# Optimization experiments

Measured on AMD Instinct MI355X. Metric: run time of the kernel, lower is better.

The kernel has to match this reference:

```python
import jax, jax.numpy as jnp
import numpy as np

EPS = 1e-5

def _act_quant(x):
    # per-token absmax int8 quantization (BitNet b1.58)
    scale = 127.0 / jnp.clip(jnp.max(jnp.abs(x), axis=-1, keepdims=True), EPS)
    return jnp.clip(jnp.round(x * scale), -128.0, 127.0) / scale

def _weight_quant(w):
    # per-tensor absmean ternary quantization {-1, 0, +1}
    scale = 1.0 / jnp.clip(jnp.mean(jnp.abs(w)), EPS)
    return jnp.clip(jnp.round(w * scale), -1.0, 1.0) / scale

def _bitlinear(x, w):
    # STE: forward uses quantized values, gradient passes through
    xq = x + jax.lax.stop_gradient(_act_quant(x) - x)
    wq = w + jax.lax.stop_gradient(_weight_quant(w) - w)
    # torch Linear: y = x @ W.T, W is [out, in]
    return jnp.einsum('bsd,od->bso', xq, wq)

def setup_inputs() -> dict:
    key = jax.random.key(0)
    k1, k2, k3, k4 = jax.random.split(key, 4)
    B, S, D = 8, 2048, 512
    x = jax.random.normal(k1, (B, S, D), dtype=jnp.float32)
    s = (1.0 / D) ** 0.5
    Wq = jax.random.normal(k2, (D, D), dtype=jnp.float32) * s
    Wk = jax.random.normal(k3, (D, D), dtype=jnp.float32) * s
    Wv = jax.random.normal(k4, (D, D), dtype=jnp.float32) * s
    return {"x": x, "Wq": Wq, "Wk": Wk, "Wv": Wv}

def reference(x, Wq, Wk, Wv):
    B, S, D = x.shape
    q = _bitlinear(x, Wq)
    k = _bitlinear(x, Wk)
    v = _bitlinear(x, Wv)
    # NOTE: original scales by batch_size**-0.5 (faithful to source)
    scores = jnp.einsum('bqd,bkd->bqk', q, k) * (B ** -0.5)
    causal = jnp.tril(jnp.ones((S, S), dtype=bool))  # tril[:S, :S]
    scores = jnp.where(causal, scores, -jnp.inf)
    attn = jax.nn.softmax(scores, axis=-1)
    return jnp.einsum('bqk,bkd->bqd', attn, v)
```

## Files before the change

### kernel.cpp

```cpp
#include <hip/hip_runtime.h>
#include <cstdint>
#include <cstddef>

#define BATCH 8
#define SEQ   2048
#define DDIM  512
#define NROW  (BATCH*SEQ)
#define KPACK (DDIM/4)
#define EPSQ  1e-5f
#define FSCALE 0.35355339059327373f

typedef _Float16 half8 __attribute__((ext_vector_type(8)));
typedef _Float16 half4 __attribute__((ext_vector_type(4)));
typedef float    f32x4 __attribute__((ext_vector_type(4)));
typedef int      i32x4 __attribute__((ext_vector_type(4)));

static constexpr size_t OFF_M   = 0;
static constexpr size_t OFF_WP  = 256;
static constexpr size_t OFF_XQ  = OFF_WP + (size_t)3*KPACK*DDIM*4;
static constexpr size_t OFF_SX  = OFF_XQ + (size_t)NROW*KPACK*4;
static constexpr size_t OFF_QKV = OFF_SX + (size_t)NROW*4;
static constexpr size_t OFF_PO  = OFF_QKV + (size_t)3*NROW*DDIM*2;
static constexpr size_t OFF_PM  = OFF_PO + (size_t)512*64*512*4;
static constexpr size_t OFF_PL  = OFF_PM + (size_t)1024*32*4;

__device__ __forceinline__ int q8(float v, float s) {
  int i = (int)rintf(v * s);
  i = i < -128 ? -128 : (i > 127 ? 127 : i);
  return i & 0xff;
}

__device__ __forceinline__ void gld_lds16(const _Float16* g, _Float16* l) {
  __builtin_amdgcn_global_load_lds(
      (const __attribute__((address_space(1))) void*)g,
      (__attribute__((address_space(3))) void*)l, 16, 0, 0);
}

__global__ __launch_bounds__(256) void wsum_kernel(
    const float* __restrict__ Wq, const float* __restrict__ Wk,
    const float* __restrict__ Wv, float* __restrict__ mw) {
  const float* W = blockIdx.y == 0 ? Wq : (blockIdx.y == 1 ? Wk : Wv);
  __shared__ float red[256];
  const float4* p = (const float4*)(W + blockIdx.x * 8192);
  float s = 0.f;
  #pragma unroll
  for (int i = 0; i < 8; i++) {
    float4 a = p[i * 256 + threadIdx.x];
    s += fabsf(a.x) + fabsf(a.y) + fabsf(a.z) + fabsf(a.w);
  }
  red[threadIdx.x] = s;
  __syncthreads();
  for (int w = 128; w > 0; w >>= 1) {
    if ((int)threadIdx.x < w) red[threadIdx.x] += red[threadIdx.x + w];
    __syncthreads();
  }
  if (threadIdx.x == 0) atomicAdd(&mw[blockIdx.y], red[0]);
}

__global__ __launch_bounds__(256) void wquant_kernel(
    const float* __restrict__ Wq, const float* __restrict__ Wk,
    const float* __restrict__ Wv, const float* __restrict__ mw,
    int* __restrict__ wp) {
  int idx = blockIdx.x * 256 + threadIdx.x;
  int mat = idx >> 16;
  int local = idx & 0xFFFF;
  int o  = local >> 7;
  int k4 = local & 127;
  const float* W = mat == 0 ? Wq : (mat == 1 ? Wk : Wv);
  float mean = mw[mat] * (1.0f / 262144.0f);
  float scale = 1.0f / fmaxf(mean, EPSQ);
  float4 w4 = *(const float4*)(W + (size_t)o * DDIM + k4 * 4);
  int t0 = (int)rintf(w4.x * scale); t0 = t0 < -1 ? -1 : (t0 > 1 ? 1 : t0);
  int t1 = (int)rintf(w4.y * scale); t1 = t1 < -1 ? -1 : (t1 > 1 ? 1 : t1);
  int t2 = (int)rintf(w4.z * scale); t2 = t2 < -1 ? -1 : (t2 > 1 ? 1 : t2);
  int t3 = (int)rintf(w4.w * scale); t3 = t3 < -1 ? -1 : (t3 > 1 ? 1 : t3);
  int packed = (t0 & 0xff) | ((t1 & 0xff) << 8) | ((t2 & 0xff) << 16) | ((t3 & 0xff) << 24);
  wp[((size_t)mat * DDIM + o) * KPACK + k4] = packed;
}

__global__ __launch_bounds__(256) void aquant_kernel(
    const float* __restrict__ x, int* __restrict__ xq, float* __restrict__ sx) {
  int wid = threadIdx.x >> 6, lane = threadIdx.x & 63;
  int row = blockIdx.x * 4 + wid;
  const float* xr = x + (size_t)row * DDIM;
  float4 a = ((const float4*)xr)[lane];
  float4 b = ((const float4*)xr)[64 + lane];
  float amax = fmaxf(fmaxf(fmaxf(fabsf(a.x), fabsf(a.y)), fmaxf(fabsf(a.z), fabsf(a.w))),
                     fmaxf(fmaxf(fabsf(b.x), fabsf(b.y)), fmaxf(fabsf(b.z), fabsf(b.w))));
  for (int off = 32; off > 0; off >>= 1) amax = fmaxf(amax, __shfl_xor(amax, off, 64));
  float aa = fmaxf(amax, EPSQ);
  float scale = 127.0f / aa;
  int p0 = q8(a.x, scale) | (q8(a.y, scale) << 8) | (q8(a.z, scale) << 16) | (q8(a.w, scale) << 24);
  int p1 = q8(b.x, scale) | (q8(b.y, scale) << 8) | (q8(b.z, scale) << 16) | (q8(b.w, scale) << 24);
  xq[(size_t)row * KPACK + lane]      = p0;
  xq[(size_t)row * KPACK + 64 + lane] = p1;
  if (lane == 0) sx[row] = aa * (1.0f / 127.0f);
}

__global__ __launch_bounds__(256, 2) void qkv_gemm_kernel(
    const int* __restrict__ xq, const int* __restrict__ wp,
    const float* __restrict__ sx, const float* __restrict__ mw,
    _Float16* __restrict__ qkv) {
  __shared__ __align__(16) int xs[64][132];
  __shared__ __align__(16) int bs[64][132];
  __shared__ float sxs[64];

  const int tid  = threadIdx.x;
  const int w    = tid >> 6;
  const int lane = tid & 63;
  const int quad = lane >> 4;
  const int col  = lane & 15;

  const int r0g = blockIdx.x * 64;
  const int n0  = blockIdx.y * 64;
  const int mat = blockIdx.z;

  {
    const i32x4* src = (const i32x4*)(xq + (size_t)r0g * KPACK);
    #pragma unroll
    for (int i = 0; i < 8; i++) {
      int e = i * 256 + tid;
      int row = e >> 5, u = e & 31;
      *(i32x4*)&xs[row][u * 4] = src[e];
    }
  }
  {
    const i32x4* src = (const i32x4*)(wp + ((size_t)mat * DDIM + n0) * KPACK);
    #pragma unroll
    for (int i = 0; i < 8; i++) {
      int e = i * 256 + tid;
      int c = e >> 5, u = e & 31;
      *(i32x4*)&bs[c][u * 4] = src[e];
    }
  }
  if (tid < 64) sxs[tid] = sx[r0g + tid];
  __syncthreads();

  i32x4 acc[4];
  #pragma unroll
  for (int rt = 0; rt < 4; rt++) acc[rt] = (i32x4)(0);

  #pragma unroll
  for (int s = 0; s < 8; s++) {
    i32x4 bf = *(const i32x4*)&bs[w * 16 + col][s * 16 + quad * 4];
    #pragma unroll
    for (int rt = 0; rt < 4; rt++) {
      i32x4 af = *(const i32x4*)&xs[rt * 16 + col][s * 16 + quad * 4];
      acc[rt] = __builtin_amdgcn_mfma_i32_16x16x64_i8(af, bf, acc[rt], 0, 0, 0);
    }
  }

  const float mval = fmaxf(mw[mat] * (1.0f / 262144.0f), EPSQ);
  const int nw = n0 + w * 16 + col;

  if (mat < 2) {
    _Float16* outb = qkv + (size_t)mat * NROW * DDIM;
    #pragma unroll
    for (int rt = 0; rt < 4; rt++) {
      #pragma unroll
      for (int reg = 0; reg < 4; reg++) {
        int rowl = rt * 16 + quad * 4 + reg;
        outb[(size_t)(r0g + rowl) * DDIM + nw] =
            (_Float16)((float)acc[rt][reg] * sxs[rowl] * mval);
      }
    }
  } else {
    _Float16* vT = qkv + (size_t)2 * NROW * DDIM;
    #pragma unroll
    for (int rt = 0; rt < 4; rt++) {
      half4 hv;
      #pragma unroll
      for (int reg = 0; reg < 4; reg++) {
        int rowl = rt * 16 + quad * 4 + reg;
        hv[reg] = (_Float16)((float)acc[rt][reg] * sxs[rowl] * mval);
      }
      int r = r0g + rt * 16 + quad * 4;
      int b = r >> 11, kt = (r & 2047) >> 5, kin = r & 31;
      *(half4*)(vT + ((((size_t)b * 64 + kt) * 512 + nw) * 32 + kin)) = hv;
    }
  }
}

__global__ __launch_bounds__(256, 2) void flash_kernel(
    const _Float16* __restrict__ q, const _Float16* __restrict__ k,
    const _Float16* __restrict__ vT, _Float16* __restrict__ po,
    float* __restrict__ pm, float* __restrict__ pl) {
  __shared__ __align__(16) _Float16 Ksh[32][520];
  __shared__ __align__(16) float    PsS[32 * 33];
  __shared__ __align__(16) _Float16 Pf[32 * 40];
  __shared__ float alpha_l[32];

  const int tid  = threadIdx.x;
  const int w    = tid >> 6;
  const int lane = tid & 63;
  const int quad = lane >> 4;
  const int col  = lane & 15;
  const int rt   = w & 1;
  const int kh   = w >> 1;
  const int smrow = tid >> 3;
  const int sme   = tid & 7;
  const int d0  = w * 128;

  const int bb = blockIdx.x & 7;
  const int r  = blockIdx.x >> 3;
  const int h  = r < 64 ? 0 : 1;
  const int qt = r < 64 ? r : 127 - r;
  const int nT = h == 0 ? (qt / 2 + 1) : ((qt + 1) / 2);
  const int slot = (qt * 8 + bb) * 2 + h;

  const int qrow0 = qt * 32;
  const size_t bbase = (size_t)bb * SEQ * DDIM;
  const _Float16* kb_p = k + bbase;
  const _Float16* vt_p = vT + (size_t)bb * 64 * 512 * 32;

  half8 qfrag[16];
  {
    const _Float16* qrow_p = q + bbase + (size_t)(qrow0 + rt * 16 + col) * DDIM;
    #pragma unroll
    for (int s = 0; s < 16; s++)
      qfrag[s] = *(const half8*)(qrow_p + s * 32 + quad * 8);
  }

  float m_run = -INFINITY, l_run = 0.f;
  f32x4 o[2][8];
  #pragma unroll
  for (int a = 0; a < 2; a++)
    #pragma unroll
    for (int b2 = 0; b2 < 8; b2++) o[a][b2] = (f32x4)(0.f);

  if (nT > 0) {
    #pragma unroll
    for (int i = 0; i < 8; i++)
      gld_lds16(kb_p + (size_t)(h * 32 + w * 8 + i) * DDIM + lane * 8,
                &Ksh[w * 8 + i][0]);
    __syncthreads();
  }

  for (int t = 0; t < nT; t++) {
    const int kt  = 2 * t + h;
    const int kb0 = kt * 32;

    {
      f32x4 c = (f32x4)(0.f);
      __builtin_amdgcn_s_setprio(1);
      #pragma unroll
      for (int s = 0; s < 16; s++) {
        half8 b = *(const half8*)&Ksh[kh * 16 + col][s * 32 + quad * 8];
        c = __builtin_amdgcn_mfma_f32_16x16x32_f16(qfrag[s], b, c, 0, 0, 0);
      }
      __builtin_amdgcn_s_setprio(0);
      #pragma unroll
      for (int reg = 0; reg < 4; reg++)
        PsS[(rt * 16 + quad * 4 + reg) * 33 + kh * 16 + col] = c[reg];
    }
    __syncthreads();

    if (t + 1 < nT) {
      const int kb1 = (2 * (t + 1) + h) * 32;
      #pragma unroll
      for (int i = 0; i < 8; i++)
        gld_lds16(kb_p + (size_t)(kb1 + w * 8 + i) * DDIM + lane * 8,
                  &Ksh[w * 8 + i][0]);
    }

    {
      const int qrow = qrow0 + smrow;
      float sv[4];
      #pragma unroll
      for (int i = 0; i < 4; i++) {
        float s = PsS[smrow * 33 + sme * 4 + i] * FSCALE;
        if (kb0 + sme * 4 + i > qrow) s = -INFINITY;
        sv[i] = s;
      }
      float mx = fmaxf(fmaxf(sv[0], sv[1]), fmaxf(sv[2], sv[3]));
      #pragma unroll
      for (int m = 1; m <= 4; m <<= 1) mx = fmaxf(mx, __shfl_xor(mx, m, 64));
      float mn = fmaxf(m_run, mx);
      float mnc = fmaxf(mn, -1e30f);
      float al = __expf(m_run - mnc);
      half4 p4;
      float rs = 0.f;
      #pragma unroll
      for (int i = 0; i < 4; i++) {
        float p = __expf(sv[i] - mnc);
        rs += p;
        p4[i] = (_Float16)p;
      }
      #pragma unroll
      for (int m = 1; m <= 4; m <<= 1) rs += __shfl_xor(rs, m, 64);
      l_run = l_run * al + rs;
      m_run = mn;
      *(half4*)&Pf[smrow * 40 + sme * 4] = p4;
      if (sme == 0) alpha_l[smrow] = al;
    }
    __syncthreads();

    {
      half8 ap[2];
      f32x4 af[2];
      #pragma unroll
      for (int r2 = 0; r2 < 2; r2++) {
        ap[r2] = *(const half8*)&Pf[(r2 * 16 + col) * 40 + quad * 8];
        af[r2] = *(const f32x4*)&alpha_l[r2 * 16 + quad * 4];
      }
      #pragma unroll
      for (int r2 = 0; r2 < 2; r2++)
        #pragma unroll
        for (int ct = 0; ct < 8; ct++)
          o[r2][ct] *= af[r2];
      const _Float16* vtile = vt_p + (size_t)kt * 512 * 32;
      __builtin_amdgcn_s_setprio(1);
      #pragma unroll
      for (int ct = 0; ct < 8; ct++) {
        int R = d0 + ct * 16 + col;
        half8 bv = *(const half8*)(vtile + (size_t)R * 32 + quad * 8);
        #pragma unroll
        for (int r2 = 0; r2 < 2; r2++)
          o[r2][ct] = __builtin_amdgcn_mfma_f32_16x16x32_f16(ap[r2], bv, o[r2][ct], 0, 0, 0);
      }
      __builtin_amdgcn_s_setprio(0);
    }
  }

  if (sme == 0) {
    pm[slot * 32 + smrow] = m_run;
    pl[slot * 32 + smrow] = l_run;
  }
  {
    _Float16* pob = po + (size_t)slot * 32 * 512;
    #pragma unroll
    for (int r2 = 0; r2 < 2; r2++) {
      #pragma unroll
      for (int ct = 0; ct < 8; ct++) {
        #pragma unroll
        for (int e = 0; e < 4; e++) {
          __builtin_nontemporal_store(
              (_Float16)o[r2][ct][e],
              &pob[(size_t)(r2 * 16 + quad * 4 + e) * 512 + d0 + ct * 16 + col]);
        }
      }
    }
  }
}

__global__ __launch_bounds__(256) void merge_kernel(
    const _Float16* __restrict__ po, const float* __restrict__ pm,
    const float* __restrict__ pl, float* __restrict__ out) {
  __shared__ float w0s[32], w1s[32], dns[32];
  const int tid = threadIdx.x;
  const int qt = blockIdx.x, b = blockIdx.y;
  const int slot0 = (qt * 8 + b) * 2;
  const int slot1 = slot0 + 1;

  if (tid < 32) {
    float m0 = pm[slot0 * 32 + tid], m1 = pm[slot1 * 32 + tid];
    float l0 = pl[slot0 * 32 + tid], l1 = pl[slot1 * 32 + tid];
    float ms = fmaxf(m0, m1);
    float a0 = __expf(m0 - ms);
    float a1 = __expf(m1 - ms);
    w0s[tid] = a0;
    w1s[tid] = a1;
    dns[tid] = 1.0f / (a0 * l0 + a1 * l1);
  }
  __syncthreads();

  const half8* p0 = (const half8*)(po + (size_t)slot0 * 32 * 512);
  const half8* p1 = (const half8*)(po + (size_t)slot1 * 32 * 512);
  f32x4* op = (f32x4*)(out + ((size_t)b * SEQ + qt * 32) * 512);
  #pragma unroll 4
  for (int j = 0; j < 8; j++) {
    int e = j * 256 + tid;
    int row = e >> 6;
    half8 a = __builtin_nontemporal_load(p0 + e);
    half8 c = __builtin_nontemporal_load(p1 + e);
    float w0 = w0s[row], w1 = w1s[row], dn = dns[row];
    f32x4 r0, r1;
    #pragma unroll
    for (int u = 0; u < 4; u++) r0[u] = ((float)a[u] * w0 + (float)c[u] * w1) * dn;
    #pragma unroll
    for (int u = 0; u < 4; u++) r1[u] = ((float)a[4 + u] * w0 + (float)c[4 + u] * w1) * dn;
    op[e * 2]     = r0;
    op[e * 2 + 1] = r1;
  }
}

extern "C" void kernel_launch(void* const* d_in, const int* in_sizes, int n_in,
                              void* d_out, int out_size, void* d_ws, size_t ws_size,
                              hipStream_t stream) {
  const float* x  = (const float*)d_in[0];
  const float* Wq = (const float*)d_in[1];
  const float* Wk = (const float*)d_in[2];
  const float* Wv = (const float*)d_in[3];
  float* out = (float*)d_out;
  char* ws = (char*)d_ws;

  float* mw  = (float*)(ws + OFF_M);
  int*   wp  = (int*)(ws + OFF_WP);
  int*   xq  = (int*)(ws + OFF_XQ);
  float* sx  = (float*)(ws + OFF_SX);
  _Float16* qkv = (_Float16*)(ws + OFF_QKV);
  _Float16* qf  = qkv;
  _Float16* kf  = qkv + (size_t)NROW * DDIM;
  _Float16* vTf = qkv + 2 * (size_t)NROW * DDIM;
  _Float16* po = (_Float16*)(ws + OFF_PO);
  float* pm = (float*)(ws + OFF_PM);
  float* pl = (float*)(ws + OFF_PL);

  hipMemsetAsync(mw, 0, 16, stream);
  wsum_kernel<<<dim3(32, 3), 256, 0, stream>>>(Wq, Wk, Wv, mw);
  wquant_kernel<<<768, 256, 0, stream>>>(Wq, Wk, Wv, mw, wp);
  aquant_kernel<<<4096, 256, 0, stream>>>(x, xq, sx);
  qkv_gemm_kernel<<<dim3(256, 8, 3), 256, 0, stream>>>(xq, wp, sx, mw, qkv);
  flash_kernel<<<dim3(1024), 256, 0, stream>>>(qf, kf, vTf, po, pm, pl);
  merge_kernel<<<dim3(64, 8), 256, 0, stream>>>(po, pm, pl, out);
}
```

Baseline: 239.4 us.

## Fuse split-KV merge into flash kernel and double-buffer swizzled K tiles

```diff
diff --git a/kernel.cpp b/kernel.cpp
--- a/kernel.cpp
+++ b/kernel.cpp
@@ -15,14 +15,15 @@
 typedef float    f32x4 __attribute__((ext_vector_type(4)));
 typedef int      i32x4 __attribute__((ext_vector_type(4)));
 
-static constexpr size_t OFF_M   = 0;
-static constexpr size_t OFF_WP  = 256;
-static constexpr size_t OFF_XQ  = OFF_WP + (size_t)3*KPACK*DDIM*4;
-static constexpr size_t OFF_SX  = OFF_XQ + (size_t)NROW*KPACK*4;
-static constexpr size_t OFF_QKV = OFF_SX + (size_t)NROW*4;
-static constexpr size_t OFF_PO  = OFF_QKV + (size_t)3*NROW*DDIM*2;
-static constexpr size_t OFF_PM  = OFF_PO + (size_t)512*64*512*4;
-static constexpr size_t OFF_PL  = OFF_PM + (size_t)1024*32*4;
+static constexpr size_t OFF_M     = 0;
+static constexpr size_t OFF_FLAGS = 64;
+static constexpr size_t OFF_WP    = 4096;
+static constexpr size_t OFF_XQ    = OFF_WP + (size_t)3*KPACK*DDIM*4;
+static constexpr size_t OFF_SX    = OFF_XQ + (size_t)NROW*KPACK*4;
+static constexpr size_t OFF_QKV   = OFF_SX + (size_t)NROW*4;
+static constexpr size_t OFF_PO    = OFF_QKV + (size_t)3*NROW*DDIM*2;
+static constexpr size_t OFF_PM    = OFF_PO + (size_t)1024*32*512*2;
+static constexpr size_t OFF_PL    = OFF_PM + (size_t)1024*32*4;
 
 __device__ __forceinline__ int q8(float v, float s) {
   int i = (int)rintf(v * s);
@@ -184,11 +185,13 @@
 __global__ __launch_bounds__(256, 2) void flash_kernel(
     const _Float16* __restrict__ q, const _Float16* __restrict__ k,
     const _Float16* __restrict__ vT, _Float16* __restrict__ po,
-    float* __restrict__ pm, float* __restrict__ pl) {
-  __shared__ __align__(16) _Float16 Ksh[32][520];
+    float* __restrict__ pm, float* __restrict__ pl,
+    int* __restrict__ flags, float* __restrict__ out) {
+  __shared__ __align__(16) _Float16 Ksh[2][32][512];
   __shared__ __align__(16) float    PsS[32 * 33];
   __shared__ __align__(16) _Float16 Pf[32 * 40];
   __shared__ float alpha_l[32];
+  __shared__ int role;
 
   const int tid  = threadIdx.x;
   const int w    = tid >> 6;
@@ -231,21 +234,38 @@
   if (nT > 0) {
     #pragma unroll
     for (int i = 0; i < 8; i++)
-      gld_lds16(kb_p + (size_t)(h * 32 + w * 8 + i) * DDIM + lane * 8,
-                &Ksh[w * 8 + i][0]);
+      gld_lds16(kb_p + (size_t)(h * 32 + w * 8 + i) * DDIM + (lane ^ i) * 8,
+                &Ksh[0][w * 8 + i][0]);
     __syncthreads();
   }
 
   for (int t = 0; t < nT; t++) {
+    const int cur = t & 1;
     const int kt  = 2 * t + h;
     const int kb0 = kt * 32;
+
+    if (t + 1 < nT) {
+      const int kb1 = (2 * t + 2 + h) * 32;
+      #pragma unroll
+      for (int i = 0; i < 8; i++)
+        gld_lds16(kb_p + (size_t)(kb1 + w * 8 + i) * DDIM + (lane ^ i) * 8,
+                  &Ksh[cur ^ 1][w * 8 + i][0]);
+    }
+    half8 vreg[8];
+    {
+      const _Float16* vtile = vt_p + (size_t)kt * 512 * 32;
+      #pragma unroll
+      for (int ct = 0; ct < 8; ct++)
+        vreg[ct] = *(const half8*)(vtile + (size_t)(d0 + ct * 16 + col) * 32 + quad * 8);
+    }
 
     {
       f32x4 c = (f32x4)(0.f);
       __builtin_amdgcn_s_setprio(1);
       #pragma unroll
       for (int s = 0; s < 16; s++) {
-        half8 b = *(const half8*)&Ksh[kh * 16 + col][s * 32 + quad * 8];
+        half8 b = *(const half8*)&Ksh[cur][kh * 16 + col]
+                                     [((s * 4 + quad) ^ (col & 7)) * 8];
         c = __builtin_amdgcn_mfma_f32_16x16x32_f16(qfrag[s], b, c, 0, 0, 0);
       }
       __builtin_amdgcn_s_setprio(0);
@@ -254,14 +274,6 @@
         PsS[(rt * 16 + quad * 4 + reg) * 33 + kh * 16 + col] = c[reg];
     }
     __syncthreads();
-
-    if (t + 1 < nT) {
-      const int kb1 = (2 * (t + 1) + h) * 32;
-      #pragma unroll
-      for (int i = 0; i < 8; i++)
-        gld_lds16(kb_p + (size_t)(kb1 + w * 8 + i) * DDIM + lane * 8,
-                  &Ksh[w * 8 + i][0]);
-    }
 
     {
       const int qrow = qrow0 + smrow;
@@ -308,16 +320,12 @@
         #pragma unroll
         for (int ct = 0; ct < 8; ct++)
           o[r2][ct] *= af[r2];
-      const _Float16* vtile = vt_p + (size_t)kt * 512 * 32;
       __builtin_amdgcn_s_setprio(1);
       #pragma unroll
-      for (int ct = 0; ct < 8; ct++) {
-        int R = d0 + ct * 16 + col;
-        half8 bv = *(const half8*)(vtile + (size_t)R * 32 + quad * 8);
+      for (int ct = 0; ct < 8; ct++)
         #pragma unroll
         for (int r2 = 0; r2 < 2; r2++)
-          o[r2][ct] = __builtin_amdgcn_mfma_f32_16x16x32_f16(ap[r2], bv, o[r2][ct], 0, 0, 0);
-      }
+          o[r2][ct] = __builtin_amdgcn_mfma_f32_16x16x32_f16(ap[r2], vreg[ct], o[r2][ct], 0, 0, 0);
       __builtin_amdgcn_s_setprio(0);
     }
   }
@@ -341,46 +349,43 @@
       }
     }
   }
-}
-
-__global__ __launch_bounds__(256) void merge_kernel(
-    const _Float16* __restrict__ po, const float* __restrict__ pm,
-    const float* __restrict__ pl, float* __restrict__ out) {
-  __shared__ float w0s[32], w1s[32], dns[32];
-  const int tid = threadIdx.x;
-  const int qt = blockIdx.x, b = blockIdx.y;
-  const int slot0 = (qt * 8 + b) * 2;
-  const int slot1 = slot0 + 1;
-
-  if (tid < 32) {
-    float m0 = pm[slot0 * 32 + tid], m1 = pm[slot1 * 32 + tid];
-    float l0 = pl[slot0 * 32 + tid], l1 = pl[slot1 * 32 + tid];
-    float ms = fmaxf(m0, m1);
-    float a0 = __expf(m0 - ms);
-    float a1 = __expf(m1 - ms);
-    w0s[tid] = a0;
-    w1s[tid] = a1;
-    dns[tid] = 1.0f / (a0 * l0 + a1 * l1);
-  }
+
+  __threadfence();
   __syncthreads();
-
-  const half8* p0 = (const half8*)(po + (size_t)slot0 * 32 * 512);
-  const half8* p1 = (const half8*)(po + (size_t)slot1 * 32 * 512);
-  f32x4* op = (f32x4*)(out + ((size_t)b * SEQ + qt * 32) * 512);
-  #pragma unroll 4
-  for (int j = 0; j < 8; j++) {
-    int e = j * 256 + tid;
-    int row = e >> 6;
-    half8 a = __builtin_nontemporal_load(p0 + e);
-    half8 c = __builtin_nontemporal_load(p1 + e);
-    float w0 = w0s[row], w1 = w1s[row], dn = dns[row];
-    f32x4 r0, r1;
-    #pragma unroll
-    for (int u = 0; u < 4; u++) r0[u] = ((float)a[u] * w0 + (float)c[u] * w1) * dn;
-    #pragma unroll
-    for (int u = 0; u < 4; u++) r1[u] = ((float)a[4 + u] * w0 + (float)c[4 + u] * w1) * dn;
-    op[e * 2]     = r0;
-    op[e * 2 + 1] = r1;
+  if (tid == 0) role = atomicAdd(&flags[slot >> 1], 1);
+  __syncthreads();
+  if (role == 1) {
+    __threadfence();
+    const int s0 = (slot >> 1) * 2, s1 = s0 + 1;
+    if (tid < 32) {
+      float m0 = pm[s0 * 32 + tid], m1 = pm[s1 * 32 + tid];
+      float l0 = pl[s0 * 32 + tid], l1 = pl[s1 * 32 + tid];
+      float ms = fmaxf(m0, m1);
+      float a0 = __expf(m0 - ms);
+      float a1 = __expf(m1 - ms);
+      PsS[tid]      = a0;
+      PsS[32 + tid] = a1;
+      PsS[64 + tid] = 1.0f / (a0 * l0 + a1 * l1);
+    }
+    __syncthreads();
+    const _Float16* psib = po + (size_t)(slot ^ 1) * 32 * 512;
+    float* outb = out + ((size_t)bb * SEQ + qrow0) * 512;
+    #pragma unroll
+    for (int r2 = 0; r2 < 2; r2++) {
+      #pragma unroll
+      for (int e = 0; e < 4; e++) {
+        const int rr = r2 * 16 + quad * 4 + e;
+        const float wown = (h == 0) ? PsS[rr] : PsS[32 + rr];
+        const float wsib = (h == 0) ? PsS[32 + rr] : PsS[rr];
+        const float dn = PsS[64 + rr];
+        #pragma unroll
+        for (int ct = 0; ct < 8; ct++) {
+          const int cc = d0 + ct * 16 + col;
+          float sv = (float)psib[(size_t)rr * 512 + cc];
+          outb[(size_t)rr * 512 + cc] = (o[r2][ct][e] * wown + sv * wsib) * dn;
+        }
+      }
+    }
   }
 }
 
@@ -395,6 +400,7 @@
   char* ws = (char*)d_ws;
 
   float* mw  = (float*)(ws + OFF_M);
+  int*   flg = (int*)(ws + OFF_FLAGS);
   int*   wp  = (int*)(ws + OFF_WP);
   int*   xq  = (int*)(ws + OFF_XQ);
   float* sx  = (float*)(ws + OFF_SX);
@@ -406,11 +412,10 @@
   float* pm = (float*)(ws + OFF_PM);
   float* pl = (float*)(ws + OFF_PL);
 
-  hipMemsetAsync(mw, 0, 16, stream);
+  hipMemsetAsync(ws, 0, 4096, stream);
   wsum_kernel<<<dim3(32, 3), 256, 0, stream>>>(Wq, Wk, Wv, mw);
   wquant_kernel<<<768, 256, 0, stream>>>(Wq, Wk, Wv, mw, wp);
   aquant_kernel<<<4096, 256, 0, stream>>>(x, xq, sx);
   qkv_gemm_kernel<<<dim3(256, 8, 3), 256, 0, stream>>>(xq, wp, sx, mw, qkv);
-  flash_kernel<<<dim3(1024), 256, 0, stream>>>(qf, kf, vTf, po, pm, pl);
-  merge_kernel<<<dim3(64, 8), 256, 0, stream>>>(po, pm, pl, out);
-}
+  flash_kernel<<<dim3(1024), 256, 0, stream>>>(qf, kf, vTf, po, pm, pl, flg, out);
+}
```

Result: slower. 468.9 us (+95.9%).
